# Kernel optimization log

Measured on AMD Instinct MI355X. Metric: run time of the kernel, lower is better.

## Reference

```python
import jax, jax.numpy as jnp
import numpy as np

N_HEADS = 16
EMBED = 1024
T = 2048        # given tokens
CACHE_NUM = 1024  # prepended cache tokens (x[0,-1] in the original)


def setup_inputs() -> dict:
    key = jax.random.key(0)
    k1, k2 = jax.random.split(key)
    qkv = jax.random.normal(k1, (T, 3 * EMBED), dtype=jnp.float32)
    # In the original these cache rows are torch.randn generated inside forward;
    # we lift them into a deterministic explicit input with identical semantics.
    cache = jax.random.normal(k2, (CACHE_NUM, 3 * EMBED), dtype=jnp.float32)
    return {"qkv": qkv, "cache": cache}


def reference(qkv, cache):
    C = EMBED
    H = N_HEADS
    D = C // H  # head_dim = 64
    t = qkv.shape[0]
    tc = cache.shape[0]
    t_full = t + tc  # T_ in the original

    gq, gk, gv = jnp.split(qkv, 3, axis=1)      # each [T, C]
    cq, ck, cv = jnp.split(cache, 3, axis=1)    # each [cache_num, C]

    q = jnp.concatenate([cq, gq], axis=0)  # [T_, C]
    k = jnp.concatenate([ck, gk], axis=0)
    v = jnp.concatenate([cv, gv], axis=0)

    # [T_, C] -> [H, T_, D]
    q = q.reshape(t_full, H, D).transpose(1, 0, 2)
    k = k.reshape(t_full, H, D).transpose(1, 0, 2)
    v = v.reshape(t_full, H, D).transpose(1, 0, 2)

    scale = 1.0 / np.sqrt(D).astype(np.float32)
    att = jnp.einsum('htd,hsd->hts', q, k) * scale  # [H, T_, T_]

    causal = jnp.tril(jnp.ones((t_full, t_full), dtype=bool))
    att = jnp.where(causal[None, :, :], att, jnp.float32(-jnp.inf))
    att = jax.nn.softmax(att, axis=-1)
    # attn_dropout is identity in eval / p=0

    y = jnp.einsum('hts,hsd->htd', att, v)          # [H, T_, D]
    y = y.transpose(1, 0, 2).reshape(t_full, C)     # [T_, C]
    return y[tc:, :]                                # drop cache rows -> [T, C]
```

## Files before the change

kernel.cpp:

```cpp
#include <hip/hip_runtime.h>
#include <cmath>


typedef _Float16 f16;
typedef __attribute__((ext_vector_type(8))) _Float16 f16x8;
typedef __attribute__((ext_vector_type(4))) _Float16 f16x4;
typedef __attribute__((ext_vector_type(2))) _Float16 f16x2;
typedef __attribute__((ext_vector_type(4))) float    f32x4;

constexpr int TC  = 1024;
constexpr int C3  = 3072;
constexpr int CE  = 1024;
constexpr int NH  = 16;
constexpr int TQ  = 2048;
constexpr int NKT = 48;

constexpr size_t KV_ELEMS = (size_t)NH * NKT * 4096;

constexpr int SPLITS[16] = {2,2,3,3,3,3,4,4,4,4,5,5,5,5,6,6};
constexpr int PRE[16]    = {0,2,4,7,10,13,16,20,24,28,32,37,42,47,52,58};
constexpr int NSLOT      = 64;

constexpr size_t OPART_E = (size_t)NSLOT * NH * 128 * 64;
constexpr size_t LPART_F = (size_t)NSLOT * NH * 128;

__device__ __forceinline__ void dma16(const void* g, void* l) {
    __builtin_amdgcn_global_load_lds(
        (const __attribute__((address_space(1))) void*)g,
        (__attribute__((address_space(3))) void*)l, 16, 0, 0);
}

__device__ __forceinline__ f16x2 pkrtz(float a, float b) {
    return __builtin_bit_cast(f16x2, __builtin_amdgcn_cvt_pkrtz(a, b));
}

__device__ __forceinline__ float fexp2(float x) {
    return __builtin_amdgcn_exp2f(x);
}

__global__ __launch_bounds__(256)
void prepass_f16(const float* __restrict__ qkv, const float* __restrict__ cache,
                 f16* __restrict__ Kt, f16* __restrict__ Vt)
{
    const int b   = blockIdx.x;
    const int h   = b & 15;
    const int kt  = b >> 4;
    const int tid = threadIdx.x;
    const int bt  = kt * 64;
    const float* src = (bt < TC) ? (cache + (size_t)bt * C3)
                                 : (qkv + (size_t)(bt - TC) * C3);
    f16* ktile = Kt + (size_t)(h * NKT + kt) * 4096;
    f16* vtile = Vt + (size_t)(h * NKT + kt) * 4096;

    __shared__ f16 vtmp[64 * 66];

    {
        const int tok = tid >> 2;
        const int c4  = tid & 3;
        const float* p = src + (size_t)tok * C3 + h * 64 + CE + c4 * 16;
        f32x4 x0 = ((const f32x4*)p)[0], x1 = ((const f32x4*)p)[1];
        f32x4 x2 = ((const f32x4*)p)[2], x3 = ((const f32x4*)p)[3];
        const int ch0 = (2 * c4)     ^ (tok & 7);
        const int ch1 = (2 * c4 + 1) ^ (tok & 7);
        *(f16x8*)&ktile[tok * 64 + ch0 * 8] =
            (f16x8){(f16)x0.x,(f16)x0.y,(f16)x0.z,(f16)x0.w,
                    (f16)x1.x,(f16)x1.y,(f16)x1.z,(f16)x1.w};
        *(f16x8*)&ktile[tok * 64 + ch1 * 8] =
            (f16x8){(f16)x2.x,(f16)x2.y,(f16)x2.z,(f16)x2.w,
                    (f16)x3.x,(f16)x3.y,(f16)x3.z,(f16)x3.w};
    }
    {
        const int tok  = tid >> 2;
        const int dblk = (tid & 3) * 16;
        const float* p = src + (size_t)tok * C3 + h * 64 + 2 * CE + dblk;
        f32x4 x0 = ((const f32x4*)p)[0], x1 = ((const f32x4*)p)[1];
        f32x4 x2 = ((const f32x4*)p)[2], x3 = ((const f32x4*)p)[3];
        float v[16] = {x0.x,x0.y,x0.z,x0.w, x1.x,x1.y,x1.z,x1.w,
                       x2.x,x2.y,x2.z,x2.w, x3.x,x3.y,x3.z,x3.w};
        f16* dst = &vtmp[tok * 66 + dblk];
        #pragma unroll
        for (int i = 0; i < 8; ++i)
            *(f16x2*)&dst[2 * i] = (f16x2){(f16)v[2 * i], (f16)v[2 * i + 1]};
    }
    __syncthreads();
    {
        const int d  = tid >> 2;
        const int tb = (tid & 3) * 16;
        f16 col[16];
        #pragma unroll
        for (int i = 0; i < 16; ++i) col[i] = vtmp[(tb + i) * 66 + d];
        const int c0 = tb >> 3;
        *(f16x8*)&vtile[d * 64 + ((c0 ^ (d & 7)) * 8)] =
            (f16x8){col[0],col[1],col[2],col[3],col[4],col[5],col[6],col[7]};
        *(f16x8*)&vtile[d * 64 + (((c0 + 1) ^ (d & 7)) * 8)] =
            (f16x8){col[8],col[9],col[10],col[11],col[12],col[13],col[14],col[15]};
    }
}

__device__ __forceinline__ void tile_loop(
    const char* kg, const char* vg, int t0, int t1, int qbase_w,
    int l15, int quad, int ksw, int soff,
    const f16x8 (&qfrag)[2][2], f16 (&sKV)[2][8192],
    f32x4 (&o_accT)[2][4], float (&l_i)[2])
{
    {
        char* kl = (char*)&sKV[0][0]    + soff;
        char* vl = (char*)&sKV[0][4096] + soff;
        dma16(kg, kl);           dma16(kg + 1024, kl + 1024);
        dma16(vg, vl);           dma16(vg + 1024, vl + 1024);
    }
    int cur = 0;

    for (int kt = t0; kt < t1; ++kt) {
        asm volatile("s_waitcnt vmcnt(0) lgkmcnt(0)" ::: "memory");
        __syncthreads();

        kg += 8192; vg += 8192;
        if (kt + 1 < t1) {
            char* kl = (char*)&sKV[cur ^ 1][0]    + soff;
            char* vl = (char*)&sKV[cur ^ 1][4096] + soff;
            dma16(kg, kl);       dma16(kg + 1024, kl + 1024);
            dma16(vg, vl);       dma16(vg + 1024, vl + 1024);
        }
        const f16* sK  = &sKV[cur][0];
        const f16* sVT = &sKV[cur][4096];
        cur ^= 1;

        f32x4 sacc[2][4];
        #pragma unroll
        for (int u = 0; u < 2; ++u)
            #pragma unroll
            for (int kb = 0; kb < 4; ++kb) sacc[u][kb] = (f32x4){0.f,0.f,0.f,0.f};
        #pragma unroll
        for (int kb = 0; kb < 4; ++kb) {
            const int ib = (kb * 16 + l15) * 64 + ksw;
            f16x8 a0 = *(const f16x8*)&sK[ib];
            f16x8 a1 = *(const f16x8*)&sK[ib ^ 32];
            #pragma unroll
            for (int u = 0; u < 2; ++u) {
                sacc[u][kb] = __builtin_amdgcn_mfma_f32_16x16x32_f16(a0, qfrag[u][0], sacc[u][kb], 0, 0, 0);
                sacc[u][kb] = __builtin_amdgcn_mfma_f32_16x16x32_f16(a1, qfrag[u][1], sacc[u][kb], 0, 0, 0);
            }
        }

        if (kt * 64 + 63 > qbase_w) {
            #pragma unroll
            for (int u = 0; u < 2; ++u) {
                const int qg = qbase_w + u * 16 + l15;
                #pragma unroll
                for (int kb = 0; kb < 4; ++kb) {
                    const int kq = kt * 64 + kb * 16 + quad * 4;
                    #pragma unroll
                    for (int r = 0; r < 4; ++r)
                        if (kq + r > qg) sacc[u][kb][r] = -INFINITY;
                }
            }
        }

        f16x4 pfrag[2][4];
        #pragma unroll
        for (int u = 0; u < 2; ++u) {
            float ls = 0.f;
            #pragma unroll
            for (int kb = 0; kb < 4; ++kb) {
                const float p0 = fexp2(sacc[u][kb][0]);
                const float p1 = fexp2(sacc[u][kb][1]);
                const float p2 = fexp2(sacc[u][kb][2]);
                const float p3 = fexp2(sacc[u][kb][3]);
                ls += (p0 + p1) + (p2 + p3);
                f16x2 lo = pkrtz(p0, p1);
                f16x2 hi = pkrtz(p2, p3);
                pfrag[u][kb] = __builtin_shufflevector(lo, hi, 0, 1, 2, 3);
            }
            l_i[u] += ls;
        }

        #pragma unroll
        for (int dblk = 0; dblk < 4; ++dblk) {
            const int row = dblk * 16 + l15;
            #pragma unroll
            for (int kb = 0; kb < 4; ++kb) {
                const int ch = (kb * 2 + (quad >> 1)) ^ (row & 7);
                f16x4 vf = *(const f16x4*)
                    &sVT[row * 64 + ch * 8 + (quad & 1) * 4];
                #pragma unroll
                for (int u = 0; u < 2; ++u)
                    o_accT[u][dblk] = __builtin_amdgcn_mfma_f32_16x16x16f16(
                        vf, pfrag[u][kb], o_accT[u][dblk], 0, 0, 0);
            }
        }
    }
}

__global__ __launch_bounds__(256, 4)
void attn_splitk(const float* __restrict__ qkv,
                 const f16* __restrict__ Kt,
                 const f16* __restrict__ Vt,
                 f16*  __restrict__ Opart,
                 float* __restrict__ lpart)
{
    const int bb = blockIdx.x;
    const int h  = bb >> 6;
    const int g  = ((bb & 63) + h * 4) & 63;
    int qt = 0;
    #pragma unroll
    for (int i = 1; i < 16; ++i) qt += (g >= PRE[i]) ? 1 : 0;
    const int s   = g - PRE[qt];
    const int nsp = SPLITS[qt];
    const int nkt = 2 * qt + 18;
    const int t0  = nkt * s / nsp;
    const int t1  = nkt * (s + 1) / nsp;

    const int tid  = threadIdx.x;
    const int w    = tid >> 6;
    const int lane = tid & 63;
    const int l15  = lane & 15;
    const int quad = lane >> 4;

    __shared__ __align__(16) f16 sKV[2][8192];

    const float qs = 0.125f * 1.44269504088896f;
    f16x8 qfrag[2][2];
    #pragma unroll
    for (int u = 0; u < 2; ++u) {
        const float* qp = qkv + (size_t)(qt * 128 + w * 32 + u * 16 + l15) * C3
                              + h * 64 + quad * 8;
        #pragma unroll
        for (int c = 0; c < 2; ++c) {
            f32x4 a = *(const f32x4*)(qp + c * 32);
            f32x4 b = *(const f32x4*)(qp + c * 32 + 4);
            qfrag[u][c] = (f16x8){(f16)(a.x * qs), (f16)(a.y * qs),
                                  (f16)(a.z * qs), (f16)(a.w * qs),
                                  (f16)(b.x * qs), (f16)(b.y * qs),
                                  (f16)(b.z * qs), (f16)(b.w * qs)};
        }
    }

    f32x4 o_accT[2][4];
    #pragma unroll
    for (int u = 0; u < 2; ++u)
        #pragma unroll
        for (int d = 0; d < 4; ++d) o_accT[u][d] = (f32x4){0.f, 0.f, 0.f, 0.f};
    float l_i[2] = {0.f, 0.f};

    const int qbase_w = TC + qt * 128 + w * 32;
    const int soff = w * 2048 + lane * 16;
    const char* kg = (const char*)(Kt + (size_t)(h * NKT + t0) * 4096) + soff;
    const char* vg = (const char*)(Vt + (size_t)(h * NKT + t0) * 4096) + soff;
    const int ksw = (quad ^ (l15 & 7)) * 8;

    tile_loop(kg, vg, t0, t1, qbase_w, l15, quad, ksw, soff,
              qfrag, sKV, o_accT, l_i);

    #pragma unroll
    for (int u = 0; u < 2; ++u) {
        float lf = l_i[u];
        lf += __shfl_xor(lf, 16);
        lf += __shfl_xor(lf, 32);
        const int qloc = w * 32 + u * 16 + l15;
        const int slot = PRE[qt] + s;
        f16*   op = Opart + ((size_t)slot * NH + h) * (128 * 64);
        float* lp = lpart + ((size_t)slot * NH + h) * 128;
        #pragma unroll
        for (int dblk = 0; dblk < 4; ++dblk) {
            f32x4 o = o_accT[u][dblk];
            f16x2 lo = pkrtz(o.x, o.y);
            f16x2 hi = pkrtz(o.z, o.w);
            *(f16x4*)&op[qloc * 64 + dblk * 16 + quad * 4] =
                __builtin_shufflevector(lo, hi, 0, 1, 2, 3);
        }
        if (quad == 0) lp[qloc] = lf;
    }
}

__global__ __launch_bounds__(256)
void attn_direct(const float* __restrict__ qkv,
                 const f16* __restrict__ Kt,
                 const f16* __restrict__ Vt,
                 float* __restrict__ out)
{
    const int bb  = blockIdx.x;
    const int h   = bb & 15;
    const int idx = bb >> 4;
    const int qt  = (h < 8) ? idx : 15 - idx;
    const int nsp = SPLITS[qt];
    const int nkt = 2 * qt + 18;

    const int tid  = threadIdx.x;
    const int w    = tid >> 6;
    const int lane = tid & 63;
    const int l15  = lane & 15;
    const int quad = lane >> 4;

    __shared__ __align__(16) f16 sKV[2][8192];

    const float qs = 0.125f * 1.44269504088896f;
    f16x8 qfrag[2][2];
    #pragma unroll
    for (int u = 0; u < 2; ++u) {
        const float* qp = qkv + (size_t)(qt * 128 + w * 32 + u * 16 + l15) * C3
                              + h * 64 + quad * 8;
        #pragma unroll
        for (int c = 0; c < 2; ++c) {
            f32x4 a = *(const f32x4*)(qp + c * 32);
            f32x4 b = *(const f32x4*)(qp + c * 32 + 4);
            qfrag[u][c] = (f16x8){(f16)(a.x * qs), (f16)(a.y * qs),
                                  (f16)(a.z * qs), (f16)(a.w * qs),
                                  (f16)(b.x * qs), (f16)(b.y * qs),
                                  (f16)(b.z * qs), (f16)(b.w * qs)};
        }
    }

    const int qbase_w = TC + qt * 128 + w * 32;
    const int soff = w * 2048 + lane * 16;
    const char* kg0 = (const char*)(Kt + (size_t)h * NKT * 4096) + soff;
    const char* vg0 = (const char*)(Vt + (size_t)h * NKT * 4096) + soff;
    const int ksw = (quad ^ (l15 & 7)) * 8;

    f32x4 osum[2][4];
    #pragma unroll
    for (int u = 0; u < 2; ++u)
        #pragma unroll
        for (int d = 0; d < 4; ++d) osum[u][d] = (f32x4){0.f, 0.f, 0.f, 0.f};
    float lsum[2] = {0.f, 0.f};

    for (int s = 0; s < nsp; ++s) {
        if (s) __syncthreads();
        const int t0 = nkt * s / nsp;
        const int t1 = nkt * (s + 1) / nsp;

        f32x4 o_accT[2][4];
        #pragma unroll
        for (int u = 0; u < 2; ++u)
            #pragma unroll
            for (int d = 0; d < 4; ++d) o_accT[u][d] = (f32x4){0.f,0.f,0.f,0.f};
        float l_i[2] = {0.f, 0.f};

        tile_loop(kg0 + (size_t)t0 * 8192, vg0 + (size_t)t0 * 8192,
                  t0, t1, qbase_w, l15, quad, ksw, soff,
                  qfrag, sKV, o_accT, l_i);

        #pragma unroll
        for (int u = 0; u < 2; ++u) {
            float lf = l_i[u];
            lf += __shfl_xor(lf, 16);
            lf += __shfl_xor(lf, 32);
            lsum[u] += lf;
            #pragma unroll
            for (int dblk = 0; dblk < 4; ++dblk) {
                f32x4 o = o_accT[u][dblk];
                f16x2 lo = pkrtz(o.x, o.y);
                f16x2 hi = pkrtz(o.z, o.w);
                osum[u][dblk].x += (float)lo[0];
                osum[u][dblk].y += (float)lo[1];
                osum[u][dblk].z += (float)hi[0];
                osum[u][dblk].w += (float)hi[1];
            }
        }
    }

    #pragma unroll
    for (int u = 0; u < 2; ++u) {
        const float inv = 1.0f / lsum[u];
        const int qloc = w * 32 + u * 16 + l15;
        const int gq = qt * 128 + qloc;
        #pragma unroll
        for (int dblk = 0; dblk < 4; ++dblk) {
            f32x4 o = osum[u][dblk];
            *(f32x4*)&out[(size_t)gq * CE + h * 64 + dblk * 16 + quad * 4] =
                (f32x4){o.x * inv, o.y * inv, o.z * inv, o.w * inv};
        }
    }
}

__global__ __launch_bounds__(256)
void combine_splits(const f16* __restrict__ Opart,
                    const float* __restrict__ lpart,
                    float* __restrict__ out)
{
    const int t  = blockIdx.x * 256 + threadIdx.x;
    const int d4 = t & 15;
    const int q  = (t >> 4) & (TQ - 1);
    const int h  = t >> 15;

    const int qt    = q >> 7;
    const int qloc  = q & 127;
    const int nsp   = SPLITS[qt];
    const int slot0 = PRE[qt];

    float lsum = 0.f;
    f32x4 acc = (f32x4){0.f, 0.f, 0.f, 0.f};
    for (int s = 0; s < nsp; ++s) {
        const size_t sb = (size_t)(slot0 + s) * NH + h;
        lsum += lpart[sb * 128 + qloc];
        f16x4 o = *(const f16x4*)&Opart[sb * (128 * 64) + qloc * 64 + d4 * 4];
        acc.x += (float)o[0]; acc.y += (float)o[1];
        acc.z += (float)o[2]; acc.w += (float)o[3];
    }
    const float inv = 1.0f / lsum;
    *(f32x4*)&out[(size_t)q * CE + h * 64 + d4 * 4] =
        (f32x4){acc.x * inv, acc.y * inv, acc.z * inv, acc.w * inv};
}

extern "C" void kernel_launch(void* const* d_in, const int* in_sizes, int n_in,
                              void* d_out, int out_size, void* d_ws, size_t ws_size,
                              hipStream_t stream)
{
    const float* qkv   = (const float*)d_in[0];
    const float* cache = (const float*)d_in[1];
    float*       out   = (float*)d_out;
    (void)in_sizes; (void)n_in; (void)out_size;

    const size_t kv_bytes = 2 * KV_ELEMS * sizeof(f16);
    const size_t need     = kv_bytes + OPART_E * sizeof(f16)
                          + LPART_F * sizeof(float);

    f16*   Kt    = (f16*)d_ws;
    f16*   Vt    = Kt + KV_ELEMS;
    f16*   Opart = (f16*)((char*)d_ws + kv_bytes);
    float* lpart = (float*)((char*)Opart + OPART_E * sizeof(f16));

    const int split = (ws_size >= need) ? 1 : 0;

    prepass_f16<<<dim3(NH * NKT), dim3(256), 0, stream>>>(qkv, cache, Kt, Vt);
    if (split) {
        attn_splitk<<<dim3(1024), dim3(256), 0, stream>>>(qkv, Kt, Vt, Opart, lpart);
        combine_splits<<<dim3(NH * TQ * 16 / 256), dim3(256), 0, stream>>>(
            Opart, lpart, out);
    } else {
        attn_direct<<<dim3(256), dim3(256), 0, stream>>>(qkv, Kt, Vt, out);
    }
}
```

Baseline: 114.5 us.

## Increase split-K granularity, re-swizzle V tile for 16-byte LDS reads, raise occupancy

Raises the per-query-tile split counts so the split-K attention launches 80 slots per head on a 2D grid, giving more, shorter blocks to balance the causal workload across CUs. The transposed V tile in LDS now uses a different XOR swizzle, so each lane fetches its four f16x4 MFMA operands with two 16-byte reads instead of four 8-byte reads. The launch-bounds occupancy hint goes from 4 to 5 blocks per CU. The finer split adds more partial outputs for the combine kernel to read and reduce, and the occupancy hint may cap registers and cause spills.

New measurement: 149.3 us. 1.3x slower.

```diff
diff --git a/kernel.cpp b/kernel.cpp
--- a/kernel.cpp
+++ b/kernel.cpp
@@ -17,9 +17,9 @@
 
 constexpr size_t KV_ELEMS = (size_t)NH * NKT * 4096;
 
-constexpr int SPLITS[16] = {2,2,3,3,3,3,4,4,4,4,5,5,5,5,6,6};
-constexpr int PRE[16]    = {0,2,4,7,10,13,16,20,24,28,32,37,42,47,52,58};
-constexpr int NSLOT      = 64;
+constexpr int SPLITS[16] = {3,3,3,4,4,4,5,5,5,5,6,6,6,7,7,7};
+constexpr int PRE[16]    = {0,3,6,9,13,17,21,26,31,36,41,47,53,59,66,73};
+constexpr int NSLOT      = 80;
 
 constexpr size_t OPART_E = (size_t)NSLOT * NH * 128 * 64;
 constexpr size_t LPART_F = (size_t)NSLOT * NH * 128;
@@ -85,14 +85,22 @@
     __syncthreads();
     {
         const int d  = tid >> 2;
-        const int tb = (tid & 3) * 16;
+        const int oq = tid & 3;
+        const int qd = oq ^ (d & 3);
+        const int d4 = (d >> 2) & 1;
         f16 col[16];
         #pragma unroll
-        for (int i = 0; i < 16; ++i) col[i] = vtmp[(tb + i) * 66 + d];
-        const int c0 = tb >> 3;
-        *(f16x8*)&vtile[d * 64 + ((c0 ^ (d & 7)) * 8)] =
+        for (int e = 0; e < 2; ++e)
+            #pragma unroll
+            for (int bb = 0; bb < 2; ++bb) {
+                const int t0 = ((e ^ d4) * 2 + bb) * 16 + qd * 4;
+                #pragma unroll
+                for (int j = 0; j < 4; ++j)
+                    col[e * 8 + bb * 4 + j] = vtmp[(t0 + j) * 66 + d];
+            }
+        *(f16x8*)&vtile[d * 64 + oq * 16] =
             (f16x8){col[0],col[1],col[2],col[3],col[4],col[5],col[6],col[7]};
-        *(f16x8*)&vtile[d * 64 + (((c0 + 1) ^ (d & 7)) * 8)] =
+        *(f16x8*)&vtile[d * 64 + oq * 16 + 8] =
             (f16x8){col[8],col[9],col[10],col[11],col[12],col[13],col[14],col[15]};
     }
 }
@@ -110,6 +118,8 @@
         dma16(vg, vl);           dma16(vg + 1024, vl + 1024);
     }
     int cur = 0;
+
+    const int sA = ((quad ^ (l15 & 3)) << 1) + ((l15 >> 2) & 1);
 
     for (int kt = t0; kt < t1; ++kt) {
         asm volatile("s_waitcnt vmcnt(0) lgkmcnt(0)" ::: "memory");
@@ -178,30 +188,33 @@
         #pragma unroll
         for (int dblk = 0; dblk < 4; ++dblk) {
             const int row = dblk * 16 + l15;
-            #pragma unroll
-            for (int kb = 0; kb < 4; ++kb) {
-                const int ch = (kb * 2 + (quad >> 1)) ^ (row & 7);
-                f16x4 vf = *(const f16x4*)
-                    &sVT[row * 64 + ch * 8 + (quad & 1) * 4];
+            f16x8 vv01 = *(const f16x8*)&sVT[row * 64 + sA * 8];
+            f16x8 vv23 = *(const f16x8*)&sVT[row * 64 + (sA ^ 1) * 8];
+            f16x4 vf[4];
+            vf[0] = __builtin_shufflevector(vv01, vv01, 0, 1, 2, 3);
+            vf[1] = __builtin_shufflevector(vv01, vv01, 4, 5, 6, 7);
+            vf[2] = __builtin_shufflevector(vv23, vv23, 0, 1, 2, 3);
+            vf[3] = __builtin_shufflevector(vv23, vv23, 4, 5, 6, 7);
+            #pragma unroll
+            for (int kb = 0; kb < 4; ++kb)
                 #pragma unroll
                 for (int u = 0; u < 2; ++u)
                     o_accT[u][dblk] = __builtin_amdgcn_mfma_f32_16x16x16f16(
-                        vf, pfrag[u][kb], o_accT[u][dblk], 0, 0, 0);
-            }
-        }
-    }
-}
-
-__global__ __launch_bounds__(256, 4)
+                        vf[kb], pfrag[u][kb], o_accT[u][dblk], 0, 0, 0);
+        }
+    }
+}
+
+__global__ __launch_bounds__(256, 5)
 void attn_splitk(const float* __restrict__ qkv,
                  const f16* __restrict__ Kt,
                  const f16* __restrict__ Vt,
                  f16*  __restrict__ Opart,
                  float* __restrict__ lpart)
 {
-    const int bb = blockIdx.x;
-    const int h  = bb >> 6;
-    const int g  = ((bb & 63) + h * 4) & 63;
+    const int h = blockIdx.y;
+    int g = blockIdx.x + h * 5;
+    if (g >= NSLOT) g -= NSLOT;
     int qt = 0;
     #pragma unroll
     for (int i = 1; i < 16; ++i) qt += (g >= PRE[i]) ? 1 : 0;
@@ -424,7 +437,8 @@
 
     prepass_f16<<<dim3(NH * NKT), dim3(256), 0, stream>>>(qkv, cache, Kt, Vt);
     if (split) {
-        attn_splitk<<<dim3(1024), dim3(256), 0, stream>>>(qkv, Kt, Vt, Opart, lpart);
+        attn_splitk<<<dim3(NSLOT, NH), dim3(256), 0, stream>>>(
+            qkv, Kt, Vt, Opart, lpart);
         combine_splits<<<dim3(NH * TQ * 16 / 256), dim3(256), 0, stream>>>(
             Opart, lpart, out);
     } else {
```
